# Kernel tuning notes

Hardware: AMD Instinct MI355X
Metric: run time of the kernel (lower is better)

Reference implementation:

```python
import jax, jax.numpy as jnp
import numpy as np

LATENT = 128   # latent_size
FDIM = 32      # feature_dim per plane
FSIZE = 512    # feature_size -> grid is (FSIZE+1)^2
HID = 256      # hidden_dim
N = 500000     # number of query points
IN_DIM = 3
G = FSIZE + 1
SDF_IN = 3 * FDIM + LATENT + IN_DIM  # 227


def setup_inputs() -> dict:
    key = jax.random.key(0)
    ks = jax.random.split(key, 6)
    x = jax.random.normal(ks[0], (N, LATENT + IN_DIM), jnp.float32)
    # 3 tri-planes, each [FDIM, G, G], init randn*0.01 as in FeaturePlanes
    P = jax.random.normal(ks[1], (3, FDIM, G, G), jnp.float32) * 0.01

    def lin(k, fan_in, fan_out):
        s = 1.0 / np.sqrt(fan_in)
        kw, kb = jax.random.split(k)
        W = jax.random.uniform(kw, (fan_in, fan_out), jnp.float32, -s, s)
        b = jax.random.uniform(kb, (fan_out,), jnp.float32, -s, s)
        return W, b

    W0, b0 = lin(ks[2], SDF_IN, HID)
    W1, b1 = lin(ks[3], HID, HID)
    W2, b2 = lin(ks[4], HID, 1)
    return dict(x=x, P=P, W0=W0, b0=b0, W1=W1, b1=b1, W2=W2, b2=b2)


def _sample_plane(plane, uv):
    """Bilinear grid_sample, align_corners=True, padding_mode='border'.
    plane: [C, G, G]; uv: [Npts, 2] with uv[:,0]->width(x), uv[:,1]->height(y).
    Returns [Npts, C]."""
    g = jnp.clip((uv + 1.0) * 0.5 * (G - 1), 0.0, G - 1)  # unnormalize + border clamp
    gx, gy = g[:, 0], g[:, 1]
    x0f, y0f = jnp.floor(gx), jnp.floor(gy)
    x0 = x0f.astype(jnp.int32)
    y0 = y0f.astype(jnp.int32)
    x1 = jnp.minimum(x0 + 1, G - 1)
    y1 = jnp.minimum(y0 + 1, G - 1)
    wx = gx - x0f
    wy = gy - y0f
    v00 = plane[:, y0, x0]  # [C, Npts]
    v01 = plane[:, y0, x1]
    v10 = plane[:, y1, x0]
    v11 = plane[:, y1, x1]
    top = v00 * (1.0 - wx) + v01 * wx
    bot = v10 * (1.0 - wx) + v11 * wx
    return (top * (1.0 - wy) + bot * wy).T  # [Npts, C]


def reference(x, P, W0, b0, W1, b1, W2, b2):
    in_latents = x[:, :LATENT]
    in_x = x[:, -3:]
    coords = jax.lax.stop_gradient(in_x)  # matches .detach() before grid_sample
    # dimension pairs (0,1), (0,2), (1,2) -> one bilinear lookup each, vmapped
    uv = jnp.stack([coords[:, [0, 1]], coords[:, [0, 2]], coords[:, [1, 2]]])  # [3,N,2]
    feats = jax.vmap(_sample_plane)(P, uv)              # [3, N, FDIM]
    feats = jnp.transpose(feats, (1, 0, 2)).reshape(x.shape[0], 3 * FDIM)
    net_in = jnp.concatenate([in_latents, in_x, feats], axis=-1)  # [N, 227]
    h = jax.nn.relu(net_in @ W0 + b0)
    h = jax.nn.relu(h @ W1 + b1)
    out = (h @ W2 + b2).squeeze(-1)  # [N]
    return out
```

## Files before the change

kernel.cpp:

```cpp
#include <hip/hip_runtime.h>
#include <stdint.h>

#define XDIM 131
#define LATENT 128
#define FDIM 32
#define GSZ 513
#define SDF_IN 227
#define FEAT0 136
#define BSTRIDE 2064

typedef __attribute__((ext_vector_type(8))) short bf16x8;
typedef __attribute__((ext_vector_type(4))) float f32x4;
typedef unsigned int uint32;

__device__ __forceinline__ unsigned short f2bf(float f) {
  uint32 u = __float_as_uint(f);
  u += 0x7fffu + ((u >> 16) & 1u);
  return (unsigned short)(u >> 16);
}
__device__ __forceinline__ float bf2f(unsigned short s) {
  return __uint_as_float(((uint32)s) << 16);
}
__device__ __forceinline__ uint32 pk2bf(float a, float b) {
  return (uint32)f2bf(a) | ((uint32)f2bf(b) << 16);
}

__device__ __forceinline__ int slot16(int r) { return (r * 16) ^ (((r >> 3) & 1) << 5); }
__device__ __forceinline__ int blk_of(int c) { return (c >> 5) * 4 + ((c >> 3) & 3); }
__device__ __forceinline__ int act_byte(int r, int c) {
  return blk_of(c) * BSTRIDE + slot16(r) + (c & 7) * 2;
}

__global__ void prep_pt(const float* __restrict__ P, unsigned short* __restrict__ Pt) {
  int i = blockIdx.x * 256 + threadIdx.x;
  const int CELLS = 3 * GSZ * GSZ;
  if (i >= CELLS) return;
  int pl = i / (GSZ * GSZ);
  int yx = i - pl * (GSZ * GSZ);
  const float* src = P + (size_t)pl * FDIM * GSZ * GSZ + yx;
  const size_t GG = (size_t)GSZ * GSZ;
  uint4* dst = (uint4*)(Pt + (size_t)i * 32);
#pragma unroll
  for (int w = 0; w < 4; ++w) {
    uint4 t;
    t.x = pk2bf(src[(w * 8 + 0) * GG], src[(w * 8 + 1) * GG]);
    t.y = pk2bf(src[(w * 8 + 2) * GG], src[(w * 8 + 3) * GG]);
    t.z = pk2bf(src[(w * 8 + 4) * GG], src[(w * 8 + 5) * GG]);
    t.w = pk2bf(src[(w * 8 + 6) * GG], src[(w * 8 + 7) * GG]);
    dst[w] = t;
  }
}

__global__ void prep_w(const float* __restrict__ W0, const float* __restrict__ W1,
                       unsigned short* __restrict__ W0g, unsigned short* __restrict__ W1g) {
  int i = blockIdx.x * 256 + threadIdx.x;
  int sel = i >> 13;
  int t = i & 8191;
  int kb = t >> 10;
  int g  = (t >> 8) & 3;
  int n  = t & 255;
  float vv[8];
#pragma unroll
  for (int j = 0; j < 8; ++j) {
    int k = kb * 32 + g * 8 + j;
    float val;
    if (sel == 0) {
      int src = (k < 131) ? k : ((k >= FEAT0 && k < FEAT0 + 96) ? k - 5 : -1);
      val = (src >= 0) ? W0[src * 256 + n] : 0.f;
    } else {
      val = W1[k * 256 + n];
    }
    vv[j] = val;
  }
  uint4 o;
  o.x = pk2bf(vv[0], vv[1]);
  o.y = pk2bf(vv[2], vv[3]);
  o.z = pk2bf(vv[4], vv[5]);
  o.w = pk2bf(vv[6], vv[7]);
  unsigned short* dst = (sel == 0 ? W0g : W1g) + (size_t)t * 8;
  *(uint4*)dst = o;
}

__device__ __forceinline__ void gemm_layer(unsigned char* actb,
                                           const unsigned short* __restrict__ Wg,
                                           const float* __restrict__ bias,
                                           int rg, int cg, int lr, int lg)
{
  f32x4 acc[4][4];
#pragma unroll
  for (int mf = 0; mf < 4; ++mf)
#pragma unroll
    for (int nf = 0; nf < 4; ++nf) acc[mf][nf] = (f32x4){0.f, 0.f, 0.f, 0.f};

  float bs[4];
#pragma unroll
  for (int nf = 0; nf < 4; ++nf) bs[nf] = bias[cg * 64 + nf * 16 + lr];

#pragma unroll
  for (int kb = 0; kb < 8; ++kb) {
    bf16x8 a[4], b[4];
    const int ab = (kb * 4 + lg) * BSTRIDE;
#pragma unroll
    for (int mf = 0; mf < 4; ++mf)
      a[mf] = *(const bf16x8*)(actb + ab + slot16(rg * 64 + mf * 16 + lr));
#pragma unroll
    for (int nf = 0; nf < 4; ++nf)
      b[nf] = *(const bf16x8*)(Wg + (size_t)(kb * 4 + lg) * 2048 + (size_t)(cg * 64 + nf * 16 + lr) * 8);
#pragma unroll
    for (int mf = 0; mf < 4; ++mf)
#pragma unroll
      for (int nf = 0; nf < 4; ++nf)
        acc[mf][nf] = __builtin_amdgcn_mfma_f32_16x16x32_bf16(a[mf], b[nf], acc[mf][nf], 0, 0, 0);
  }
  __syncthreads();
#pragma unroll
  for (int mf = 0; mf < 4; ++mf)
#pragma unroll
    for (int nf = 0; nf < 4; ++nf) {
      int c = cg * 64 + nf * 16 + lr;
      unsigned char* dst = actb + blk_of(c) * BSTRIDE + (c & 7) * 2;
#pragma unroll
      for (int reg = 0; reg < 4; ++reg) {
        int r = rg * 64 + mf * 16 + lg * 4 + reg;
        float vv = fmaxf(acc[mf][nf][reg] + bs[nf], 0.f);
        *(unsigned short*)(dst + slot16(r)) = f2bf(vv);
      }
    }
  __syncthreads();
}

template<int USE_PT>
__global__ __launch_bounds__(512, 4) void sdf_main(
    const float* __restrict__ x, const float* __restrict__ P,
    const unsigned short* __restrict__ Pt,
    const unsigned short* __restrict__ W0g, const unsigned short* __restrict__ W1g,
    const float* __restrict__ b0, const float* __restrict__ b1,
    const float* __restrict__ W2, const float* __restrict__ b2v,
    float* __restrict__ out, int Npts)
{
  __shared__ __align__(16) unsigned char actb[32 * BSTRIDE];

  const int tid = threadIdx.x;
  const int p0 = blockIdx.x * 128;

  for (int z = tid; z < 516; z += 512) {
    uint4 zz = {0u, 0u, 0u, 0u};
    if (z < 129) ((uint4*)(actb + 16 * BSTRIDE))[z] = zz;
    else         ((uint4*)(actb + 29 * BSTRIDE))[z - 129] = zz;
  }
  __syncthreads();

#pragma unroll
  for (int i = 0; i < 4; ++i) {
    int t = i * 512 + tid;
    int cb = t & 15, r = t >> 4;
    int p = min(p0 + r, Npts - 1);
    const float* src = x + (size_t)p * XDIM + cb * 8;
    uint4 v;
    v.x = pk2bf(src[0], src[1]);
    v.y = pk2bf(src[2], src[3]);
    v.z = pk2bf(src[4], src[5]);
    v.w = pk2bf(src[6], src[7]);
    *(uint4*)(actb + cb * BSTRIDE + slot16(r)) = v;
  }
  if (tid < 128) {
    int r = tid;
    int p = min(p0 + r, Npts - 1);
#pragma unroll
    for (int j = 0; j < 3; ++j)
      *(unsigned short*)(actb + act_byte(r, 128 + j)) = f2bf(x[(size_t)p * XDIM + 128 + j]);
  }

  {
    int p_l = tid >> 2;
    int q = tid & 3;
    int p = min(p0 + p_l, Npts - 1);
    const float* xr = x + (size_t)p * XDIM + LATENT;
    float cc0 = xr[0], cc1 = xr[1], cc2 = xr[2];
#pragma unroll
    for (int pl = 0; pl < 3; ++pl) {
      float u = (pl == 2) ? cc1 : cc0;
      float v = (pl == 0) ? cc1 : cc2;
      float gx = fminf(fmaxf((u + 1.f) * 256.f, 0.f), 512.f);
      float gy = fminf(fmaxf((v + 1.f) * 256.f, 0.f), 512.f);
      float x0f = floorf(gx), y0f = floorf(gy);
      int x0 = (int)x0f, y0 = (int)y0f;
      int x1 = min(x0 + 1, GSZ - 1), y1 = min(y0 + 1, GSZ - 1);
      float wx = gx - x0f, wy = gy - y0f;
      float w00 = (1.f - wx) * (1.f - wy), w01 = wx * (1.f - wy);
      float w10 = (1.f - wx) * wy,        w11 = wx * wy;
      const unsigned short* pb = Pt + (size_t)pl * GSZ * GSZ * 32 + q * 8;
      bf16x8 v00 = *(const bf16x8*)(pb + (size_t)(y0 * GSZ + x0) * 32);
      bf16x8 v01 = *(const bf16x8*)(pb + (size_t)(y0 * GSZ + x1) * 32);
      bf16x8 v10 = *(const bf16x8*)(pb + (size_t)(y1 * GSZ + x0) * 32);
      bf16x8 v11 = *(const bf16x8*)(pb + (size_t)(y1 * GSZ + x1) * 32);
      float f[8];
#pragma unroll
      for (int j = 0; j < 8; ++j) {
        f[j] = w00 * bf2f((unsigned short)v00[j])
             + w01 * bf2f((unsigned short)v01[j])
             + w10 * bf2f((unsigned short)v10[j])
             + w11 * bf2f((unsigned short)v11[j]);
      }
      uint4 fv;
      fv.x = pk2bf(f[0], f[1]);
      fv.y = pk2bf(f[2], f[3]);
      fv.z = pk2bf(f[4], f[5]);
      fv.w = pk2bf(f[6], f[7]);
      *(uint4*)(actb + (17 + pl * 4 + q) * BSTRIDE + slot16(p_l)) = fv;
    }
  }
  __syncthreads();

  const int lane = tid & 63, wid = tid >> 6;
  const int rg = wid >> 2, cg = wid & 3, lr = lane & 15, lg = lane >> 4;

  gemm_layer(actb, W0g, b0, rg, cg, lr, lg);
  gemm_layer(actb, W1g, b1, rg, cg, lr, lg);

  {
    int p_l = tid >> 2, q = tid & 3;
    float sum = 0.f;
#pragma unroll 2
    for (int m = 0; m < 8; ++m) {
      int cbase = m * 32 + q * 8;
      bf16x8 h = *(const bf16x8*)(actb + (m * 4 + q) * BSTRIDE + slot16(p_l));
      float4 wa = *(const float4*)(W2 + cbase);
      float4 wb = *(const float4*)(W2 + cbase + 4);
      sum += bf2f((unsigned short)h[0]) * wa.x + bf2f((unsigned short)h[1]) * wa.y
           + bf2f((unsigned short)h[2]) * wa.z + bf2f((unsigned short)h[3]) * wa.w
           + bf2f((unsigned short)h[4]) * wb.x + bf2f((unsigned short)h[5]) * wb.y
           + bf2f((unsigned short)h[6]) * wb.z + bf2f((unsigned short)h[7]) * wb.w;
    }
    sum += __shfl_xor(sum, 1);
    sum += __shfl_xor(sum, 2);
    if (q == 0) {
      int p = p0 + p_l;
      if (p < Npts) out[p] = sum + b2v[0];
    }
  }
}

extern "C" void kernel_launch(void* const* d_in, const int* in_sizes, int n_in,
                              void* d_out, int out_size, void* d_ws, size_t ws_size,
                              hipStream_t stream)
{
  const float* x  = (const float*)d_in[0];
  const float* P  = (const float*)d_in[1];
  const float* W0 = (const float*)d_in[2];
  const float* b0 = (const float*)d_in[3];
  const float* W1 = (const float*)d_in[4];
  const float* b1 = (const float*)d_in[5];
  const float* W2 = (const float*)d_in[6];
  const float* b2 = (const float*)d_in[7];
  float* out = (float*)d_out;
  int Npts = in_sizes[0] / XDIM;

  const size_t PT_BYTES = (size_t)3 * GSZ * GSZ * 32 * 2;
  const size_t WG_BYTES = (size_t)8192 * 8 * 2;
  char* ws = (char*)d_ws;
  int use_pt = (ws_size >= PT_BYTES + 2 * WG_BYTES) ? 1 : 0;
  unsigned short *Ptb, *W0g, *W1g;
  if (use_pt) {
    Ptb = (unsigned short*)ws;
    W0g = (unsigned short*)(ws + PT_BYTES);
    W1g = (unsigned short*)(ws + PT_BYTES + WG_BYTES);
  } else {
    Ptb = nullptr;
    W0g = (unsigned short*)ws;
    W1g = (unsigned short*)(ws + WG_BYTES);
  }

  prep_w<<<64, 256, 0, stream>>>(W0, W1, W0g, W1g);
  if (use_pt) prep_pt<<<(3 * GSZ * GSZ + 255) / 256, 256, 0, stream>>>(P, Ptb);

  int nblk = (Npts + 127) / 128;
  if (use_pt)
    sdf_main<1><<<nblk, 512, 0, stream>>>(x, P, Ptb, W0g, W1g, b0, b1, W2, b2, out, Npts);
  else
    sdf_main<0><<<nblk, 512, 0, stream>>>(x, P, Ptb, W0g, W1g, b0, b1, W2, b2, out, Npts);
}
```

Measured before the change: 328.2 us.

## Halve point tile to 64 rows with 256-thread blocks and stream B fragments

Reduces the per-block point tile from 128 to 64 and the block size from 512 to 256 threads, so each wave covers all rows and a 64-column slice. The LDS activation buffer shrinks by half, allowing more resident blocks per CU and better latency hiding. The GEMM inner loop now loads one weight fragment at a time and applies it across all M fragments, cutting live registers. The trade-off is twice as many blocks each rereading the full weight matrices from L2.

```diff
diff --git a/kernel.cpp b/kernel.cpp
--- a/kernel.cpp
+++ b/kernel.cpp
@@ -7,7 +7,8 @@
 #define GSZ 513
 #define SDF_IN 227
 #define FEAT0 136
-#define BSTRIDE 2064
+#define TROWS 64
+#define BSTRIDE 1040
 
 typedef __attribute__((ext_vector_type(8))) short bf16x8;
 typedef __attribute__((ext_vector_type(4))) float f32x4;
@@ -84,7 +85,7 @@
 __device__ __forceinline__ void gemm_layer(unsigned char* actb,
                                            const unsigned short* __restrict__ Wg,
                                            const float* __restrict__ bias,
-                                           int rg, int cg, int lr, int lg)
+                                           int cg, int lr, int lg)
 {
   f32x4 acc[4][4];
 #pragma unroll
@@ -98,19 +99,19 @@
 
 #pragma unroll
   for (int kb = 0; kb < 8; ++kb) {
-    bf16x8 a[4], b[4];
+    bf16x8 a[4];
     const int ab = (kb * 4 + lg) * BSTRIDE;
 #pragma unroll
     for (int mf = 0; mf < 4; ++mf)
-      a[mf] = *(const bf16x8*)(actb + ab + slot16(rg * 64 + mf * 16 + lr));
-#pragma unroll
-    for (int nf = 0; nf < 4; ++nf)
-      b[nf] = *(const bf16x8*)(Wg + (size_t)(kb * 4 + lg) * 2048 + (size_t)(cg * 64 + nf * 16 + lr) * 8);
-#pragma unroll
-    for (int mf = 0; mf < 4; ++mf)
-#pragma unroll
-      for (int nf = 0; nf < 4; ++nf)
-        acc[mf][nf] = __builtin_amdgcn_mfma_f32_16x16x32_bf16(a[mf], b[nf], acc[mf][nf], 0, 0, 0);
+      a[mf] = *(const bf16x8*)(actb + ab + slot16(mf * 16 + lr));
+    const unsigned short* wb = Wg + (size_t)(kb * 4 + lg) * 2048 + (size_t)(cg * 64 + lr) * 8;
+#pragma unroll
+    for (int nf = 0; nf < 4; ++nf) {
+      bf16x8 b = *(const bf16x8*)(wb + nf * 128);
+#pragma unroll
+      for (int mf = 0; mf < 4; ++mf)
+        acc[mf][nf] = __builtin_amdgcn_mfma_f32_16x16x32_bf16(a[mf], b, acc[mf][nf], 0, 0, 0);
+    }
   }
   __syncthreads();
 #pragma unroll
@@ -121,7 +122,7 @@
       unsigned char* dst = actb + blk_of(c) * BSTRIDE + (c & 7) * 2;
 #pragma unroll
       for (int reg = 0; reg < 4; ++reg) {
-        int r = rg * 64 + mf * 16 + lg * 4 + reg;
+        int r = mf * 16 + lg * 4 + reg;
         float vv = fmaxf(acc[mf][nf][reg] + bs[nf], 0.f);
         *(unsigned short*)(dst + slot16(r)) = f2bf(vv);
       }
@@ -130,7 +131,7 @@
 }
 
 template<int USE_PT>
-__global__ __launch_bounds__(512, 4) void sdf_main(
+__global__ __launch_bounds__(256, 4) void sdf_main(
     const float* __restrict__ x, const float* __restrict__ P,
     const unsigned short* __restrict__ Pt,
     const unsigned short* __restrict__ W0g, const unsigned short* __restrict__ W1g,
@@ -141,18 +142,18 @@
   __shared__ __align__(16) unsigned char actb[32 * BSTRIDE];
 
   const int tid = threadIdx.x;
-  const int p0 = blockIdx.x * 128;
-
-  for (int z = tid; z < 516; z += 512) {
+  const int p0 = blockIdx.x * TROWS;
+
+  for (int z = tid; z < 260; z += 256) {
     uint4 zz = {0u, 0u, 0u, 0u};
-    if (z < 129) ((uint4*)(actb + 16 * BSTRIDE))[z] = zz;
-    else         ((uint4*)(actb + 29 * BSTRIDE))[z - 129] = zz;
-  }
-  __syncthreads();
-
-#pragma unroll
+    if (z < 65) ((uint4*)(actb + 16 * BSTRIDE))[z] = zz;
+    else        ((uint4*)(actb + 29 * BSTRIDE))[z - 65] = zz;
+  }
+  __syncthreads();
+
+#pragma unroll 1
   for (int i = 0; i < 4; ++i) {
-    int t = i * 512 + tid;
+    int t = i * 256 + tid;
     int cb = t & 15, r = t >> 4;
     int p = min(p0 + r, Npts - 1);
     const float* src = x + (size_t)p * XDIM + cb * 8;
@@ -163,7 +164,7 @@
     v.w = pk2bf(src[6], src[7]);
     *(uint4*)(actb + cb * BSTRIDE + slot16(r)) = v;
   }
-  if (tid < 128) {
+  if (tid < TROWS) {
     int r = tid;
     int p = min(p0 + r, Npts - 1);
 #pragma unroll
@@ -213,10 +214,10 @@
   __syncthreads();
 
   const int lane = tid & 63, wid = tid >> 6;
-  const int rg = wid >> 2, cg = wid & 3, lr = lane & 15, lg = lane >> 4;
-
-  gemm_layer(actb, W0g, b0, rg, cg, lr, lg);
-  gemm_layer(actb, W1g, b1, rg, cg, lr, lg);
+  const int lr = lane & 15, lg = lane >> 4;
+
+  gemm_layer(actb, W0g, b0, wid, lr, lg);
+  gemm_layer(actb, W1g, b1, wid, lr, lg);
 
   {
     int p_l = tid >> 2, q = tid & 3;
@@ -274,9 +275,9 @@
   prep_w<<<64, 256, 0, stream>>>(W0, W1, W0g, W1g);
   if (use_pt) prep_pt<<<(3 * GSZ * GSZ + 255) / 256, 256, 0, stream>>>(P, Ptb);
 
-  int nblk = (Npts + 127) / 128;
+  int nblk = (Npts + TROWS - 1) / TROWS;
   if (use_pt)
-    sdf_main<1><<<nblk, 512, 0, stream>>>(x, P, Ptb, W0g, W1g, b0, b1, W2, b2, out, Npts);
+    sdf_main<1><<<nblk, 256, 0, stream>>>(x, P, Ptb, W0g, W1g, b0, b1, W2, b2, out, Npts);
   else
-    sdf_main<0><<<nblk, 512, 0, stream>>>(x, P, Ptb, W0g, W1g, b0, b1, W2, b2, out, Npts);
-}
+    sdf_main<0><<<nblk, 256, 0, stream>>>(x, P, Ptb, W0g, W1g, b0, b1, W2, b2, out, Npts);
+}
```

Measured after the change: 333.7 us. Within noise of the previous version (+1.7%).
